# Optimization experiments

Hardware: AMD Instinct MI355X
Metric: run time of the kernel (lower is better)

Reference implementation:

```python
import jax, jax.numpy as jnp
import numpy as np

PSP_SIZES = (1, 3, 6, 8)  # KV length S = 1 + 9 + 36 + 64 = 110
BN_EPS = 1e-5


def conv1x1(x, W, b):
    # x: [B,C,H,W], W: [O,C], b: [O] -> [B,O,H,W]
    return jnp.einsum('bchw,oc->bohw', x, W) + b[None, :, None, None]


def psp(f):
    # f: [B,C,H,W] -> [B,C,S]; H,W divisible by all sizes so adaptive pool == block mean
    B, C, H, W = f.shape
    priors = []
    for s in PSP_SIZES:
        p = f.reshape(B, C, s, H // s, s, W // s).mean(axis=(3, 5))  # [B,C,s,s]
        priors.append(p.reshape(B, C, s * s))
    return jnp.concatenate(priors, axis=-1)  # [B,C,S]


def setup_inputs() -> dict:
    key = jax.random.key(0)
    ks = jax.random.split(key, 8)
    B, C, H, W = 8, 512, 72, 72
    Kc, Vc = 256, 256
    return {
        'x': jax.random.normal(ks[0], (B, C, H, W), jnp.float32),
        'Wk': jax.random.normal(ks[1], (Kc, C), jnp.float32) * (1.0 / np.sqrt(C)),
        'bk': jax.random.normal(ks[2], (Kc,), jnp.float32) * 0.01,
        'gamma': jnp.ones((Kc,), jnp.float32),
        'beta': jnp.zeros((Kc,), jnp.float32),
        'rmean': jnp.zeros((Kc,), jnp.float32),
        'rvar': jax.random.uniform(ks[3], (Kc,), jnp.float32, 0.5, 1.5),
        'Wv': jax.random.normal(ks[4], (Vc, C), jnp.float32) * (1.0 / np.sqrt(C)),
        'bv': jax.random.normal(ks[5], (Vc,), jnp.float32) * 0.01,
        'Ww': jax.random.normal(ks[6], (C, Vc), jnp.float32) * (1.0 / np.sqrt(Vc)),
        'bw': jnp.zeros((C,), jnp.float32),
    }


def reference(x, Wk, bk, gamma, beta, rmean, rvar, Wv, bv, Ww, bw):
    B, C, H, W = x.shape
    Kc = Wk.shape[0]
    Vc = Wv.shape[0]
    # f_value: conv1x1, then PSP -> value [B,S,Vc]
    value = psp(conv1x1(x, Wv, bv)).transpose(0, 2, 1)
    # f_key == f_query: conv1x1 + BN(inference) + ReLU
    k = conv1x1(x, Wk, bk)
    inv = gamma / jnp.sqrt(rvar + BN_EPS)
    k = jax.nn.relu(k * inv[None, :, None, None] + (beta - rmean * inv)[None, :, None, None])
    query = k.reshape(B, Kc, H * W).transpose(0, 2, 1)  # [B,HW,Kc]
    keyt = psp(k)  # [B,Kc,S]
    sim = jnp.einsum('bnk,bks->bns', query, keyt) * (Kc ** -0.5)
    sim = jax.nn.softmax(sim, axis=-1)
    context = jnp.einsum('bns,bsv->bnv', sim, value)  # [B,HW,Vc]
    context = context.transpose(0, 2, 1).reshape(B, Vc, H, W)
    return conv1x1(context, Ww, bw)
```

## Files before the change

### kernel.cpp

```cpp
#include <hip/hip_runtime.h>
#include <hip/hip_bf16.h>

#define HW    5184
#define WIDTH 72
#define CIN   512
#define KC    256
#define VC    256
#define NS    110
#define NSP   112
#define SPV   128
#define BATCH 8

typedef unsigned short u16;
typedef unsigned int   u32;
typedef __attribute__((ext_vector_type(8))) short bf16x8;
typedef __attribute__((ext_vector_type(4))) float f32x4;

typedef const __attribute__((address_space(1))) u32* gp_t;
typedef __attribute__((address_space(3))) u32* lp_t;

__device__ __forceinline__ u32 f2bf1(float f) {
    u32 u = __float_as_uint(f);
    return (u + 0x7FFFu + ((u >> 16) & 1u)) >> 16;
}
__device__ __forceinline__ u32 pack2(float a, float b) {
    return f2bf1(a) | (f2bf1(b) << 16);
}

__global__ void prep_kernel(const float* __restrict__ bk, const float* __restrict__ gamma,
                            const float* __restrict__ beta, const float* __restrict__ rmean,
                            const float* __restrict__ rvar, float* __restrict__ inv_out,
                            float* __restrict__ bc_out) {
    int i = threadIdx.x;
    float inv = gamma[i] * rsqrtf(rvar[i] + 1e-5f);
    inv_out[i] = inv;
    bc_out[i]  = bk[i] * inv + beta[i] - rmean[i] * inv;
}

__global__ __launch_bounds__(256) void cvt_w_kernel(
    const float* __restrict__ Wk, const float* __restrict__ Ww, const float* __restrict__ Wv,
    u16* __restrict__ Wkbf, u16* __restrict__ Wwbf, u16* __restrict__ Wvbf)
{
    int j = (blockIdx.x * 256 + threadIdx.x) * 4;
    const float* s; u16* d;
    if (j < KC * CIN)          { s = Wk; d = Wkbf; }
    else if (j < 2 * KC * CIN) { j -= KC * CIN;     s = Ww; d = Wwbf; }
    else                       { j -= 2 * KC * CIN; s = Wv; d = Wvbf; }
    float4 v = *(const float4*)&s[j];
    uint2 u;
    u.x = pack2(v.x, v.y);
    u.y = pack2(v.z, v.w);
    *(uint2*)&d[j] = u;
}

__global__ __launch_bounds__(256) void transpose_cvt_kernel(
    const float* __restrict__ in, u16* __restrict__ out, int C)
{
    const int z  = blockIdx.z;
    const int n0 = blockIdx.x * 64;
    const int k0 = blockIdx.y * 64;
    __shared__ float t[64][65];
    const int tx = threadIdx.x & 63, ty = threadIdx.x >> 6;
    const float* src = in + ((size_t)z * C + k0) * HW + n0;
#pragma unroll
    for (int i = 0; i < 16; i++)
        t[ty + i * 4][tx] = src[(size_t)(ty + i * 4) * HW + tx];
    __syncthreads();
    u16* dst = out + ((size_t)z * HW + n0) * C + k0;
    const int kp  = (threadIdx.x & 31) * 2;
    const int nl0 = threadIdx.x >> 5;
#pragma unroll
    for (int j = 0; j < 8; j++) {
        int nl = nl0 + j * 8;
        u32 u = pack2(t[kp][nl], t[kp + 1][nl]);
        *(u32*)&dst[(size_t)nl * C + kp] = u;
    }
}

__global__ __launch_bounds__(256) void gemm_nt_bf16(
    const u16* __restrict__ A, const u16* __restrict__ B, float* __restrict__ C,
    u16* __restrict__ Ct,
    int M, int N, int K, int nbx, int nby,
    const float* __restrict__ scale, const float* __restrict__ bias, int relu)
{
    const int tot = nbx * nby * BATCH;
    const int q = tot >> 3, r = tot & 7;
    const int xcd = blockIdx.x & 7;
    const int wg  = (xcd < r ? xcd * (q + 1) : r * (q + 1) + (xcd - r) * q) + (blockIdx.x >> 3);
    const int mb_ = wg % nby;
    const int nb_ = (wg / nby) % nbx;
    const int z   = wg / (nby * nbx);

    const int n0 = nb_ * 128;
    const int m0 = mb_ * 128;
    const size_t boff = (size_t)z * N * K;
    const size_t coff = (size_t)z * M * N;
    const int tid  = threadIdx.x;
    const int wid  = tid >> 6;
    const int lane = tid & 63;

    __shared__ __align__(16) u16 As[3][4][128][8];
    __shared__ __align__(16) u16 Bs[3][4][128][8];

    const int kg0  = (wid & 1) * 2;
    const int half = (wid >> 1) * 64;

    const u16* gA = A + (size_t)(m0 + half + lane) * K + kg0 * 8;
    int nIdx = n0 + half + lane;
    if (nIdx > N - 1) nIdx = N - 1;
    const u16* gB = B + boff + (size_t)nIdx * K + kg0 * 8;

    const int wm  = (wid >> 1) * 64;
    const int wn  = (wid & 1) * 64;
    const int l16 = lane & 15;
    const int lq  = lane >> 4;

    f32x4 acc[4][4];
#pragma unroll
    for (int mi = 0; mi < 4; mi++)
#pragma unroll
        for (int ni = 0; ni < 4; ni++)
            acc[mi][ni] = (f32x4){0.f, 0.f, 0.f, 0.f};

#define STAGE(d, kk)                                                                              \
    __builtin_amdgcn_global_load_lds((gp_t)(gA + (kk)),     (lp_t)&As[d][kg0][half][0], 16, 0, 0);\
    __builtin_amdgcn_global_load_lds((gp_t)(gA + (kk) + 8), (lp_t)&As[d][kg0+1][half][0],16, 0, 0);\
    __builtin_amdgcn_global_load_lds((gp_t)(gB + (kk)),     (lp_t)&Bs[d][kg0][half][0], 16, 0, 0);\
    __builtin_amdgcn_global_load_lds((gp_t)(gB + (kk) + 8), (lp_t)&Bs[d][kg0+1][half][0],16, 0, 0);

    const int NT = K >> 5;
    STAGE(0, 0)
    STAGE(1, 32)

    int cur = 0;
    for (int t = 0; t < NT; ++t) {
        if (t + 1 < NT) { asm volatile("s_waitcnt vmcnt(4)" ::: "memory"); }
        else            { asm volatile("s_waitcnt vmcnt(0)" ::: "memory"); }
        __builtin_amdgcn_s_barrier();
        __builtin_amdgcn_sched_barrier(0);

        if (t + 2 < NT) {
            int nb = cur + 2; if (nb >= 3) nb -= 3;
            STAGE(nb, (t + 2) * 32)
        }

        bf16x8 af[4], bf[4];
#pragma unroll
        for (int i = 0; i < 4; i++) {
            af[i] = *(const bf16x8*)&As[cur][lq][wm + i * 16 + l16][0];
            bf[i] = *(const bf16x8*)&Bs[cur][lq][wn + i * 16 + l16][0];
        }
        __builtin_amdgcn_s_setprio(1);
#pragma unroll
        for (int mi = 0; mi < 4; mi++)
#pragma unroll
            for (int ni = 0; ni < 4; ni++)
                acc[mi][ni] = __builtin_amdgcn_mfma_f32_16x16x32_bf16(
                    af[mi], bf[ni], acc[mi][ni], 0, 0, 0);
        __builtin_amdgcn_s_setprio(0);

        cur = (cur == 2) ? 0 : cur + 1;
    }
#undef STAGE

#pragma unroll
    for (int mi = 0; mi < 4; mi++) {
        const int mb = m0 + wm + mi * 16 + lq * 4;
        float sc[4], bi[4];
#pragma unroll
        for (int r2 = 0; r2 < 4; r2++) {
            sc[r2] = scale ? scale[mb + r2] : 1.0f;
            bi[r2] = bias  ? bias[mb + r2]  : 0.0f;
        }
#pragma unroll
        for (int ni = 0; ni < 4; ni++) {
            const int n = n0 + wn + ni * 16 + l16;
            if (n < N) {
                float v[4];
#pragma unroll
                for (int r2 = 0; r2 < 4; r2++) {
                    v[r2] = acc[mi][ni][r2] * sc[r2] + bi[r2];
                    if (relu) v[r2] = fmaxf(v[r2], 0.f);
                    C[coff + (size_t)(mb + r2) * N + n] = v[r2];
                }
                if (Ct) {
                    uint2 u;
                    u.x = pack2(v[0], v[1]);
                    u.y = pack2(v[2], v[3]);
                    *(uint2*)&Ct[(size_t)z * N * M + (size_t)n * M + mb] = u;
                }
            }
        }
    }
}

__global__ __launch_bounds__(256) void value_mfma_kernel(
    const u16* __restrict__ A, const u16* __restrict__ Bp,
    const float* __restrict__ bv, u16* __restrict__ valT)
{
    const int m0 = blockIdx.x * 128;
    const int b  = blockIdx.y;
    const int tid  = threadIdx.x;
    const int wid  = tid >> 6;
    const int lane = tid & 63;

    __shared__ __align__(16) u16 As[4][128][8];
    __shared__ __align__(16) u16 Bs[4][128][8];

    const int kg0  = (wid & 1) * 2;
    const int half = (wid >> 1) * 64;

    const u16* gA = A + (size_t)(m0 + half + lane) * CIN + kg0 * 8;
    const u16* gB = Bp + (size_t)b * SPV * CIN + (size_t)(half + lane) * CIN + kg0 * 8;

    lp_t lA0 = (lp_t)&As[kg0][half][0];
    lp_t lA1 = (lp_t)&As[kg0 + 1][half][0];
    lp_t lB0 = (lp_t)&Bs[kg0][half][0];
    lp_t lB1 = (lp_t)&Bs[kg0 + 1][half][0];

    const int wm  = (wid >> 1) * 64;
    const int wn  = (wid & 1) * 64;
    const int l16 = lane & 15;
    const int lq  = lane >> 4;

    f32x4 acc[4][4];
#pragma unroll
    for (int mi = 0; mi < 4; mi++)
#pragma unroll
        for (int ni = 0; ni < 4; ni++)
            acc[mi][ni] = (f32x4){0.f, 0.f, 0.f, 0.f};

    for (int k0 = 0; k0 < CIN; k0 += 32) {
        __builtin_amdgcn_global_load_lds((gp_t)(gA + k0),     lA0, 16, 0, 0);
        __builtin_amdgcn_global_load_lds((gp_t)(gA + k0 + 8), lA1, 16, 0, 0);
        __builtin_amdgcn_global_load_lds((gp_t)(gB + k0),     lB0, 16, 0, 0);
        __builtin_amdgcn_global_load_lds((gp_t)(gB + k0 + 8), lB1, 16, 0, 0);
        __syncthreads();

        bf16x8 af[4], bf[4];
#pragma unroll
        for (int i = 0; i < 4; i++) {
            af[i] = *(const bf16x8*)&As[lq][wm + i * 16 + l16][0];
            bf[i] = *(const bf16x8*)&Bs[lq][wn + i * 16 + l16][0];
        }
#pragma unroll
        for (int mi = 0; mi < 4; mi++)
#pragma unroll
            for (int ni = 0; ni < 4; ni++)
                acc[mi][ni] = __builtin_amdgcn_mfma_f32_16x16x32_bf16(
                    af[mi], bf[ni], acc[mi][ni], 0, 0, 0);
        __syncthreads();
    }

    char* vb = (char*)valT + (size_t)b * VC * SPV * 2;
#pragma unroll
    for (int mi = 0; mi < 4; mi++) {
        const int mb = m0 + wm + mi * 16 + lq * 4;
        float bi[4];
#pragma unroll
        for (int r = 0; r < 4; r++) bi[r] = bv[mb + r];
#pragma unroll
        for (int ni = 0; ni < 4; ni++) {
            const int n = wn + ni * 16 + l16;
#pragma unroll
            for (int r = 0; r < 4; r++) {
                const int v = mb + r;
                const int byte = v * 256 + ((n * 2) ^ ((v & 7) << 4));
                *(u16*)(vb + byte) = (u16)f2bf1(acc[mi][ni][r] + bi[r]);
            }
        }
    }
}

__global__ __launch_bounds__(128) void psp_pool_px_kernel(
    const float* __restrict__ in, u16* __restrict__ out)
{
    const int c = blockIdx.x;
    const int b = blockIdx.y;
    const int t = threadIdx.x;
    __shared__ float4 row4[1296];
    __shared__ float aux[100];
    float* row = (float*)row4;
    const float* src = in + ((size_t)b * CIN + c) * HW;
    for (int idx = t; idx < 1296; idx += 128)
        row4[idx] = *(const float4*)(src + idx * 4);
    __syncthreads();
    if (t < 64) {
        int r0 = (t >> 3) * 9, c0 = (t & 7) * 9;
        float s = 0.f;
        for (int i = 0; i < 9; i++)
            for (int j = 0; j < 9; j++) s += row[(r0 + i) * WIDTH + c0 + j];
        aux[t] = s;
    } else if (t < 100) {
        int tt = t - 64;
        int r0 = (tt / 6) * 12, c0 = (tt % 6) * 12;
        float s = 0.f;
        for (int i = 0; i < 12; i++)
            for (int j = 0; j < 12; j++) s += row[(r0 + i) * WIDTH + c0 + j];
        aux[64 + tt] = s;
    }
    __syncthreads();
    u16* ob = out + (size_t)b * SPV * CIN + c;
    if (t < 64) ob[(size_t)(46 + t) * CIN] = (u16)f2bf1(aux[t] * (1.f / 81.f));
    if (t < 36) ob[(size_t)(10 + t) * CIN] = (u16)f2bf1(aux[64 + t] * (1.f / 144.f));
    if (t < 9) {
        int r = t / 3, cc = t % 3;
        float s4 = aux[64 + (2 * r) * 6 + 2 * cc] + aux[64 + (2 * r) * 6 + 2 * cc + 1]
                 + aux[64 + (2 * r + 1) * 6 + 2 * cc] + aux[64 + (2 * r + 1) * 6 + 2 * cc + 1];
        ob[(size_t)(1 + t) * CIN] = (u16)f2bf1(s4 * (1.f / 576.f));
    }
    if (t == 0) {
        float s = 0.f;
        for (int i = 0; i < 64; i++) s += aux[i];
        ob[0] = (u16)f2bf1(s * (1.f / 5184.f));
    }
    if (t < 18) ob[(size_t)(110 + t) * CIN] = 0;
}

__global__ __launch_bounds__(128) void psp_pool_bf16_kernel(
    const float* __restrict__ in, u16* __restrict__ out)
{
    const int c = blockIdx.x;
    const int b = blockIdx.y;
    const int t = threadIdx.x;
    __shared__ float4 row4[1296];
    __shared__ float aux[100];
    float* row = (float*)row4;
    const float* src = in + ((size_t)b * KC + c) * HW;
    for (int idx = t; idx < 1296; idx += 128)
        row4[idx] = *(const float4*)(src + idx * 4);
    __syncthreads();
    if (t < 64) {
        int r0 = (t >> 3) * 9, c0 = (t & 7) * 9;
        float s = 0.f;
        for (int i = 0; i < 9; i++)
            for (int j = 0; j < 9; j++) s += row[(r0 + i) * WIDTH + c0 + j];
        aux[t] = s;
    } else if (t < 100) {
        int tt = t - 64;
        int r0 = (tt / 6) * 12, c0 = (tt % 6) * 12;
        float s = 0.f;
        for (int i = 0; i < 12; i++)
            for (int j = 0; j < 12; j++) s += row[(r0 + i) * WIDTH + c0 + j];
        aux[64 + tt] = s;
    }
    __syncthreads();
    char* ob = (char*)out + (size_t)b * NSP * KC * 2;
    const int c2 = c * 2;
#define KWR(S, V) *(u16*)(ob + (S) * 512 + (c2 ^ (((S) & 7) << 4))) = (u16)f2bf1(V)
    if (t < 64) KWR(46 + t, aux[t] * (1.f / 81.f));
    if (t < 36) KWR(10 + t, aux[64 + t] * (1.f / 144.f));
    if (t < 9) {
        int r = t / 3, cc = t % 3;
        float s4 = aux[64 + (2 * r) * 6 + 2 * cc] + aux[64 + (2 * r) * 6 + 2 * cc + 1]
                 + aux[64 + (2 * r + 1) * 6 + 2 * cc] + aux[64 + (2 * r + 1) * 6 + 2 * cc + 1];
        KWR(1 + t, s4 * (1.f / 576.f));
    }
    if (t == 0) {
        float s = 0.f;
        for (int i = 0; i < 64; i++) s += aux[i];
        KWR(0, s * (1.f / 5184.f));
        KWR(110, 0.f);
        KWR(111, 0.f);
    }
#undef KWR
}

__global__ __launch_bounds__(256, 2) void attn_mfma_kernel(
    const u16* __restrict__ qT, const u16* __restrict__ keyt,
    const u16* __restrict__ valT, const u16* __restrict__ Wwb,
    const float* __restrict__ bw, float* __restrict__ out)
{
    const int b    = blockIdx.y;
    const int tid  = threadIdx.x;
    const int wid  = tid >> 6;
    const int lane = tid & 63;
    const int l16  = lane & 15;
    const int lq   = lane >> 4;
    const int nblk = blockIdx.x * 64;
    const int px0  = nblk + wid * 16;

    __shared__ __align__(16) u16 SM[40960];
    char* base = (char*)SM;
    const int VBUF = 32768;
    const int POFF = 65536;

    const char* gk = (const char*)keyt + (size_t)b * (NSP * KC * 2);
    const char* gv = (const char*)valT + (size_t)b * (VC * SPV * 2);

#pragma unroll
    for (int i = 0; i < 8; i++) {
        const int o = (wid * 8 + i) * 1024;
        __builtin_amdgcn_global_load_lds((gp_t)(gk + o + lane * 16), (lp_t)(base + o), 16, 0, 0);
    }
#pragma unroll
    for (int i = 0; i < 8; i++) {
        const int o = (wid * 8 + i) * 1024;
        __builtin_amdgcn_global_load_lds((gp_t)(gv + o + lane * 16), (lp_t)(base + VBUF + o), 16, 0, 0);
    }

    const u16* qrow = qT + ((size_t)b * HW + px0 + l16) * KC + lq * 8;
    bf16x8 aq[8];
#pragma unroll
    for (int ks = 0; ks < 8; ks++) aq[ks] = *(const bf16x8*)(qrow + ks * 32);

    __syncthreads();

    f32x4 acc[7];
#pragma unroll
    for (int ni = 0; ni < 7; ni++) acc[ni] = (f32x4){0.f, 0.f, 0.f, 0.f};
#pragma unroll
    for (int ks = 0; ks < 8; ks++) {
#pragma unroll
        for (int ni = 0; ni < 4; ni++) {
            const int s = ni * 16 + l16;
            const int byte = s * 512 + ((ks * 64 + lq * 16) ^ ((s & 7) << 4));
            bf16x8 bk = *(const bf16x8*)(base + byte);
            acc[ni] = __builtin_amdgcn_mfma_f32_16x16x32_bf16(aq[ks], bk, acc[ni], 0, 0, 0);
        }
    }
    __syncthreads();

#pragma unroll
    for (int i = 0; i < 6; i++) {
        const int o = (wid * 6 + i) * 1024;
        __builtin_amdgcn_global_load_lds((gp_t)(gk + 32768 + o + lane * 16), (lp_t)(base + o), 16, 0, 0);
    }
    __syncthreads();

#pragma unroll
    for (int ks = 0; ks < 8; ks++) {
#pragma unroll
        for (int ni = 4; ni < 7; ni++) {
            const int s = ni * 16 + l16;
            const int srow = s - 64;
            const int byte = srow * 512 + ((ks * 64 + lq * 16) ^ ((srow & 7) << 4));
            bf16x8 bk = *(const bf16x8*)(base + byte);
            acc[ni] = __builtin_amdgcn_mfma_f32_16x16x32_bf16(aq[ks], bk, acc[ni], 0, 0, 0);
        }
    }
    if (l16 >= 14) acc[6] = (f32x4){-1e30f, -1e30f, -1e30f, -1e30f};

    float mx[4], sm[4], rn[4];
#pragma unroll
    for (int r = 0; r < 4; r++) {
        float m = acc[0][r];
#pragma unroll
        for (int ni = 1; ni < 7; ni++) m = fmaxf(m, acc[ni][r]);
        m = fmaxf(m, __shfl_xor(m, 1));
        m = fmaxf(m, __shfl_xor(m, 2));
        m = fmaxf(m, __shfl_xor(m, 4));
        m = fmaxf(m, __shfl_xor(m, 8));
        mx[r] = m * 0.0625f;
        sm[r] = 0.f;
    }

    const int prow = wid * 16 + 4 * lq;
#pragma unroll
    for (int ni = 0; ni < 7; ni++) {
#pragma unroll
        for (int r = 0; r < 4; r++) {
            float p = __expf(acc[ni][r] * 0.0625f - mx[r]);
            sm[r] += p;
            const int row = prow + r;
            const int byte = POFF + row * 256 + (((ni * 16 + l16) * 2) ^ ((row & 7) << 4));
            *(u16*)(base + byte) = (u16)f2bf1(p);
        }
    }
    if (l16 < 2) {
#pragma unroll
        for (int r = 0; r < 4; r++) {
            const int row = prow + r;
            const int byte = POFF + row * 256 + ((224 + l16 * 16) ^ ((row & 7) << 4));
            *(bf16x8*)(base + byte) = (bf16x8){0, 0, 0, 0, 0, 0, 0, 0};
        }
    }
#pragma unroll
    for (int r = 0; r < 4; r++) {
        float s = sm[r];
        s += __shfl_xor(s, 1);
        s += __shfl_xor(s, 2);
        s += __shfl_xor(s, 4);
        s += __shfl_xor(s, 8);
        rn[r] = 1.f / s;
    }

    f32x4 acc2[16];
#pragma unroll
    for (int ni = 0; ni < 16; ni++) acc2[ni] = (f32x4){0.f, 0.f, 0.f, 0.f};
    const int arow = wid * 16 + l16;
    const int aswz = (arow & 7) << 4;
#pragma unroll
    for (int ks = 0; ks < 4; ks++) {
        const int pbyte = POFF + arow * 256 + ((ks * 64 + lq * 16) ^ aswz);
        bf16x8 pa = *(const bf16x8*)(base + pbyte);
#pragma unroll
        for (int ni = 0; ni < 8; ni++) {
            const int v = ni * 16 + l16;
            const int vbyte = VBUF + v * 256 + ((ks * 64 + lq * 16) ^ ((v & 7) << 4));
            bf16x8 bvv = *(const bf16x8*)(base + vbyte);
            acc2[ni] = __builtin_amdgcn_mfma_f32_16x16x32_bf16(pa, bvv, acc2[ni], 0, 0, 0);
        }
    }
    __syncthreads();

#pragma unroll
    for (int i = 0; i < 8; i++) {
        const int o = (wid * 8 + i) * 1024;
        __builtin_amdgcn_global_load_lds((gp_t)(gv + 32768 + o + lane * 16), (lp_t)(base + VBUF + o), 16, 0, 0);
    }
    __syncthreads();

#pragma unroll
    for (int ks = 0; ks < 4; ks++) {
        const int pbyte = POFF + arow * 256 + ((ks * 64 + lq * 16) ^ aswz);
        bf16x8 pa = *(const bf16x8*)(base + pbyte);
#pragma unroll
        for (int ni = 8; ni < 16; ni++) {
            const int vrow = (ni - 8) * 16 + l16;
            const int vbyte = VBUF + vrow * 256 + ((ks * 64 + lq * 16) ^ ((vrow & 7) << 4));
            bf16x8 bvv = *(const bf16x8*)(base + vbyte);
            acc2[ni] = __builtin_amdgcn_mfma_f32_16x16x32_bf16(pa, bvv, acc2[ni], 0, 0, 0);
        }
    }
    __syncthreads();

#pragma unroll
    for (int ni = 0; ni < 16; ni++) {
#pragma unroll
        for (int r = 0; r < 4; r++) {
            const int row = prow + r;
            const int v = ni * 16 + l16;
            const int byte = row * 512 + ((v * 2) ^ ((row & 7) << 4));
            *(u16*)(base + byte) = (u16)f2bf1(acc2[ni][r] * rn[r]);
        }
    }
    __syncthreads();

    const int wc0 = wid * 128;
    f32x4 accg[4][8];
#pragma unroll
    for (int pi = 0; pi < 4; pi++)
#pragma unroll
        for (int cj = 0; cj < 8; cj++)
            accg[pi][cj] = (f32x4){0.f, 0.f, 0.f, 0.f};

    const u16* wwbase = Wwb + (size_t)(wc0 + l16) * VC + lq * 8;
#pragma unroll
    for (int ks = 0; ks < 8; ks++) {
        bf16x8 af[4];
#pragma unroll
        for (int pi = 0; pi < 4; pi++) {
            const int px = pi * 16 + l16;
            const int byte = px * 512 + ((ks * 64 + lq * 16) ^ ((px & 7) << 4));
            af[pi] = *(const bf16x8*)(base + byte);
        }
        bf16x8 bfr[8];
#pragma unroll
        for (int cj = 0; cj < 8; cj++)
            bfr[cj] = *(const bf16x8*)(wwbase + (size_t)cj * 16 * VC + ks * 32);
#pragma unroll
        for (int pi = 0; pi < 4; pi++)
#pragma unroll
            for (int cj = 0; cj < 8; cj++)
                accg[pi][cj] = __builtin_amdgcn_mfma_f32_16x16x32_bf16(
                    af[pi], bfr[cj], accg[pi][cj], 0, 0, 0);
    }

    char* scr = base + VBUF + wid * 8192;
    float* outb = out + (size_t)b * CIN * HW + nblk;
#pragma unroll
    for (int ci = 0; ci < 4; ci++) {
#pragma unroll
        for (int cjh = 0; cjh < 2; cjh++) {
            const int cj = ci * 2 + cjh;
            const int cl = cjh * 16 + l16;
            const int swz = (cl & 7) << 5;
#pragma unroll
            for (int pi = 0; pi < 4; pi++)
#pragma unroll
                for (int r = 0; r < 4; r++) {
                    const int px = pi * 16 + 4 * lq + r;
                    *(float*)(scr + cl * 256 + ((px * 4) ^ swz)) = accg[pi][cj][r];
                }
        }
#pragma unroll
        for (int cr = 0; cr < 8; cr++) {
            const int cl = cr * 4 + lq;
            const int swz = (cl & 7) << 5;
            float4 vv = *(const float4*)(scr + cl * 256 + ((l16 * 16) ^ swz));
            const int c = wc0 + ci * 32 + cl;
            const float bb = bw[c];
            vv.x += bb; vv.y += bb; vv.z += bb; vv.w += bb;
            *(float4*)&outb[(size_t)c * HW + l16 * 4] = vv;
        }
    }
}

extern "C" void kernel_launch(void* const* d_in, const int* in_sizes, int n_in,
                              void* d_out, int out_size, void* d_ws, size_t ws_size,
                              hipStream_t stream)
{
    const float* x     = (const float*)d_in[0];
    const float* Wk    = (const float*)d_in[1];
    const float* bk    = (const float*)d_in[2];
    const float* gamma = (const float*)d_in[3];
    const float* beta  = (const float*)d_in[4];
    const float* rmean = (const float*)d_in[5];
    const float* rvar  = (const float*)d_in[6];
    const float* Wv    = (const float*)d_in[7];
    const float* bv    = (const float*)d_in[8];
    const float* Ww    = (const float*)d_in[9];
    const float* bw    = (const float*)d_in[10];
    float* out = (float*)d_out;

    float* ws    = (float*)d_ws;
    float* k_ws  = ws;
    u16*   xT    = (u16*)(k_ws + (size_t)BATCH * KC * HW);
    u16*   kT    = xT + (size_t)BATCH * HW * CIN;
    u16*   pxb   = kT + (size_t)BATCH * HW * KC;
    u16*   keytb = pxb + (size_t)BATCH * SPV * CIN;
    u16*   valT  = keytb + (size_t)BATCH * NSP * KC;
    u16*   Wkbf  = valT + (size_t)BATCH * VC * SPV;
    u16*   Wwbf  = Wkbf + (size_t)KC * CIN;
    u16*   Wvbf  = Wwbf + (size_t)CIN * VC;
    float* inv   = (float*)(Wvbf + (size_t)KC * CIN);
    float* bc    = inv + 256;

    prep_kernel<<<1, 256, 0, stream>>>(bk, gamma, beta, rmean, rvar, inv, bc);
    cvt_w_kernel<<<384, 256, 0, stream>>>(Wk, Ww, Wv, Wkbf, Wwbf, Wvbf);
    psp_pool_px_kernel<<<dim3(CIN, BATCH), 128, 0, stream>>>(x, pxb);
    transpose_cvt_kernel<<<dim3(HW / 64, CIN / 64, BATCH), 256, 0, stream>>>(x, xT, CIN);
    {
        const int nbx = (HW + 127) / 128, nby = KC / 128;
        gemm_nt_bf16<<<nbx * nby * BATCH, 256, 0, stream>>>(
            Wkbf, xT, k_ws, kT, KC, HW, CIN, nbx, nby, inv, bc, 1);
    }
    psp_pool_bf16_kernel<<<dim3(KC, BATCH), 128, 0, stream>>>(k_ws, keytb);
    value_mfma_kernel<<<dim3(2, BATCH), 256, 0, stream>>>(Wvbf, pxb, bv, valT);
    attn_mfma_kernel<<<dim3(HW / 64, BATCH), 256, 0, stream>>>(
        kT, keytb, valT, Wwbf, bw, out);
}
```

Before: 177.0 us.

## Shrink LDS footprint and register use to fit three blocks per CU

The attention kernel's shared memory drops from 80KB to 48KB. The value tile is loaded into the same buffer as the key tile once the QK^T MMAs finish, which adds extra barriers, and the output-conv scratch moves into the P region. The final Ww projection is split into two 64-channel halves, which halves the accumulator register array. Launch bounds rise to 3 blocks per SM, aiming for more occupancy to hide latency. In exchange the value load no longer overlaps the first GEMM, and there are more syncs and serialized chunks.

Measured after the change: 162.7 us. -8.1%, faster.

```diff
diff --git a/kernel.cpp b/kernel.cpp
--- a/kernel.cpp
+++ b/kernel.cpp
@@ -366,7 +366,7 @@
 #undef KWR
 }
 
-__global__ __launch_bounds__(256, 2) void attn_mfma_kernel(
+__global__ __launch_bounds__(256, 3) void attn_mfma_kernel(
     const u16* __restrict__ qT, const u16* __restrict__ keyt,
     const u16* __restrict__ valT, const u16* __restrict__ Wwb,
     const float* __restrict__ bw, float* __restrict__ out)
@@ -380,10 +380,9 @@
     const int nblk = blockIdx.x * 64;
     const int px0  = nblk + wid * 16;
 
-    __shared__ __align__(16) u16 SM[40960];
+    __shared__ __align__(16) u16 SM[24576];
     char* base = (char*)SM;
-    const int VBUF = 32768;
-    const int POFF = 65536;
+    const int POFF = 32768;
 
     const char* gk = (const char*)keyt + (size_t)b * (NSP * KC * 2);
     const char* gv = (const char*)valT + (size_t)b * (VC * SPV * 2);
@@ -392,11 +391,6 @@
     for (int i = 0; i < 8; i++) {
         const int o = (wid * 8 + i) * 1024;
         __builtin_amdgcn_global_load_lds((gp_t)(gk + o + lane * 16), (lp_t)(base + o), 16, 0, 0);
-    }
-#pragma unroll
-    for (int i = 0; i < 8; i++) {
-        const int o = (wid * 8 + i) * 1024;
-        __builtin_amdgcn_global_load_lds((gp_t)(gv + o + lane * 16), (lp_t)(base + VBUF + o), 16, 0, 0);
     }
 
     const u16* qrow = qT + ((size_t)b * HW + px0 + l16) * KC + lq * 8;
@@ -440,6 +434,13 @@
         }
     }
     if (l16 >= 14) acc[6] = (f32x4){-1e30f, -1e30f, -1e30f, -1e30f};
+    __syncthreads();
+
+#pragma unroll
+    for (int i = 0; i < 8; i++) {
+        const int o = (wid * 8 + i) * 1024;
+        __builtin_amdgcn_global_load_lds((gp_t)(gv + o + lane * 16), (lp_t)(base + o), 16, 0, 0);
+    }
 
     float mx[4], sm[4], rn[4];
 #pragma unroll
@@ -484,6 +485,7 @@
         s += __shfl_xor(s, 8);
         rn[r] = 1.f / s;
     }
+    __syncthreads();
 
     f32x4 acc2[16];
 #pragma unroll
@@ -497,7 +499,7 @@
 #pragma unroll
         for (int ni = 0; ni < 8; ni++) {
             const int v = ni * 16 + l16;
-            const int vbyte = VBUF + v * 256 + ((ks * 64 + lq * 16) ^ ((v & 7) << 4));
+            const int vbyte = v * 256 + ((ks * 64 + lq * 16) ^ ((v & 7) << 4));
             bf16x8 bvv = *(const bf16x8*)(base + vbyte);
             acc2[ni] = __builtin_amdgcn_mfma_f32_16x16x32_bf16(pa, bvv, acc2[ni], 0, 0, 0);
         }
@@ -507,7 +509,7 @@
 #pragma unroll
     for (int i = 0; i < 8; i++) {
         const int o = (wid * 8 + i) * 1024;
-        __builtin_amdgcn_global_load_lds((gp_t)(gv + 32768 + o + lane * 16), (lp_t)(base + VBUF + o), 16, 0, 0);
+        __builtin_amdgcn_global_load_lds((gp_t)(gv + 32768 + o + lane * 16), (lp_t)(base + o), 16, 0, 0);
     }
     __syncthreads();
 
@@ -518,7 +520,7 @@
 #pragma unroll
         for (int ni = 8; ni < 16; ni++) {
             const int vrow = (ni - 8) * 16 + l16;
-            const int vbyte = VBUF + vrow * 256 + ((ks * 64 + lq * 16) ^ ((vrow & 7) << 4));
+            const int vbyte = vrow * 256 + ((ks * 64 + lq * 16) ^ ((vrow & 7) << 4));
             bf16x8 bvv = *(const bf16x8*)(base + vbyte);
             acc2[ni] = __builtin_amdgcn_mfma_f32_16x16x32_bf16(pa, bvv, acc2[ni], 0, 0, 0);
         }
@@ -538,43 +540,43 @@
     __syncthreads();
 
     const int wc0 = wid * 128;
-    f32x4 accg[4][8];
-#pragma unroll
-    for (int pi = 0; pi < 4; pi++)
-#pragma unroll
-        for (int cj = 0; cj < 8; cj++)
-            accg[pi][cj] = (f32x4){0.f, 0.f, 0.f, 0.f};
-
-    const u16* wwbase = Wwb + (size_t)(wc0 + l16) * VC + lq * 8;
-#pragma unroll
-    for (int ks = 0; ks < 8; ks++) {
-        bf16x8 af[4];
-#pragma unroll
-        for (int pi = 0; pi < 4; pi++) {
-            const int px = pi * 16 + l16;
-            const int byte = px * 512 + ((ks * 64 + lq * 16) ^ ((px & 7) << 4));
-            af[pi] = *(const bf16x8*)(base + byte);
-        }
-        bf16x8 bfr[8];
-#pragma unroll
-        for (int cj = 0; cj < 8; cj++)
-            bfr[cj] = *(const bf16x8*)(wwbase + (size_t)cj * 16 * VC + ks * 32);
+    float* outb = out + (size_t)b * CIN * HW + nblk;
+    char* scr = base + POFF + wid * 4096;
+
+#pragma unroll
+    for (int ch = 0; ch < 2; ch++) {
+        f32x4 accg[4][4];
 #pragma unroll
         for (int pi = 0; pi < 4; pi++)
 #pragma unroll
-            for (int cj = 0; cj < 8; cj++)
-                accg[pi][cj] = __builtin_amdgcn_mfma_f32_16x16x32_bf16(
-                    af[pi], bfr[cj], accg[pi][cj], 0, 0, 0);
-    }
-
-    char* scr = base + VBUF + wid * 8192;
-    float* outb = out + (size_t)b * CIN * HW + nblk;
-#pragma unroll
-    for (int ci = 0; ci < 4; ci++) {
-#pragma unroll
-        for (int cjh = 0; cjh < 2; cjh++) {
-            const int cj = ci * 2 + cjh;
-            const int cl = cjh * 16 + l16;
+            for (int cj = 0; cj < 4; cj++)
+                accg[pi][cj] = (f32x4){0.f, 0.f, 0.f, 0.f};
+
+        const u16* wwbase = Wwb + (size_t)(wc0 + ch * 64 + l16) * VC + lq * 8;
+#pragma unroll
+        for (int ks = 0; ks < 8; ks++) {
+            bf16x8 af[4];
+#pragma unroll
+            for (int pi = 0; pi < 4; pi++) {
+                const int px = pi * 16 + l16;
+                const int byte = px * 512 + ((ks * 64 + lq * 16) ^ ((px & 7) << 4));
+                af[pi] = *(const bf16x8*)(base + byte);
+            }
+            bf16x8 bfr[4];
+#pragma unroll
+            for (int cj = 0; cj < 4; cj++)
+                bfr[cj] = *(const bf16x8*)(wwbase + (size_t)cj * 16 * VC + ks * 32);
+#pragma unroll
+            for (int pi = 0; pi < 4; pi++)
+#pragma unroll
+                for (int cj = 0; cj < 4; cj++)
+                    accg[pi][cj] = __builtin_amdgcn_mfma_f32_16x16x32_bf16(
+                        af[pi], bfr[cj], accg[pi][cj], 0, 0, 0);
+        }
+
+#pragma unroll
+        for (int cj = 0; cj < 4; cj++) {
+            const int cl = l16;
             const int swz = (cl & 7) << 5;
 #pragma unroll
             for (int pi = 0; pi < 4; pi++)
@@ -583,16 +585,16 @@
                     const int px = pi * 16 + 4 * lq + r;
                     *(float*)(scr + cl * 256 + ((px * 4) ^ swz)) = accg[pi][cj][r];
                 }
-        }
-#pragma unroll
-        for (int cr = 0; cr < 8; cr++) {
-            const int cl = cr * 4 + lq;
-            const int swz = (cl & 7) << 5;
-            float4 vv = *(const float4*)(scr + cl * 256 + ((l16 * 16) ^ swz));
-            const int c = wc0 + ci * 32 + cl;
-            const float bb = bw[c];
-            vv.x += bb; vv.y += bb; vv.z += bb; vv.w += bb;
-            *(float4*)&outb[(size_t)c * HW + l16 * 4] = vv;
+#pragma unroll
+            for (int cr = 0; cr < 4; cr++) {
+                const int cl2 = cr * 4 + lq;
+                const int swz2 = (cl2 & 7) << 5;
+                float4 vv = *(const float4*)(scr + cl2 * 256 + ((l16 * 16) ^ swz2));
+                const int c = wc0 + ch * 64 + cj * 16 + cl2;
+                const float bb = bw[c];
+                vv.x += bb; vv.y += bb; vv.z += bb; vv.w += bb;
+                *(float4*)&outb[(size_t)c * HW + l16 * 4] = vv;
+            }
         }
     }
 }
```
